# Kernel optimization log

Hardware: AMD Instinct MI355X
Metric: run time of the kernel (lower is better)

The kernel has to match this reference:

```python
import jax, jax.numpy as jnp
import numpy as np

EPSILON = float(np.finfo(np.float32).tiny)
K = 32                 # self.k
TRAIN_ENSEMBLE = 2     # repeat_sample in train mode
TAU = 0.1


def setup_inputs() -> dict:
    key = jax.random.key(0)
    scores = jax.random.normal(key, (256, 8192, 4), dtype=jnp.float32)  # [bsz, Nmax, ensemble]
    return {"scores": scores}


def reference(scores):
    bsz, Nmax, ensemble = scores.shape
    repeat = TRAIN_ENSEMBLE
    local_k = min(K, Nmax)

    # flat_scores: (bsz*ensemble, Nmax), then repeated over samples -> (repeat*bsz*ensemble, Nmax)
    flat = scores.transpose(0, 2, 1).reshape(bsz * ensemble, Nmax)
    flat = jnp.tile(flat, (repeat, 1))

    # Gumbel(0,1) noise (m.sample())
    g = jax.random.gumbel(jax.random.key(42), flat.shape, dtype=flat.dtype)
    flat = flat + g

    zeros = jnp.zeros_like(flat)

    def step(carry, _):
        f, khot, onehot = carry
        khot_mask = jnp.maximum(1.0 - onehot, EPSILON)
        f = f + jnp.log(khot_mask)
        onehot = jax.nn.softmax(f / TAU, axis=1)
        return (f, khot + onehot, onehot), None

    (_, khot, _), _ = jax.lax.scan(step, (flat, zeros, zeros), None, length=local_k)

    # hard top-k straight-through
    _, ind = jax.lax.top_k(khot, local_k)                      # (R, local_k)
    rows = jnp.arange(khot.shape[0])[:, None]
    khot_hard = jnp.zeros_like(khot).at[rows, ind].set(1.0)
    res = khot_hard - jax.lax.stop_gradient(khot) + khot

    # (repeat, bsz, ensemble, Nmax) -> (repeat, bsz, Nmax, ensemble)
    new_mask = res.reshape(repeat, bsz, ensemble, Nmax).transpose(0, 1, 3, 2)
    return new_mask
```

## Files before the change

kernel.cpp:

```cpp
#include <hip/hip_runtime.h>

#define TPB 256
#define ROWN 8192
#define CMAX 1024
#define EPS_TINY 1.1754943508222875e-38f

__device__ __forceinline__ unsigned rotl32(unsigned x, int r) {
  return (x << r) | (x >> (32 - r));
}

__device__ __forceinline__ unsigned tf_pxor(unsigned idx) {
  const unsigned ks0 = 0u, ks1 = 42u, ks2 = 0x1BD11BDAu ^ 0u ^ 42u;
  unsigned x0 = ks0;
  unsigned x1 = idx + ks1;
#define TF4(a,b,cc,d) \
  x0 += x1; x1 = rotl32(x1,(a));  x1 ^= x0; \
  x0 += x1; x1 = rotl32(x1,(b));  x1 ^= x0; \
  x0 += x1; x1 = rotl32(x1,(cc)); x1 ^= x0; \
  x0 += x1; x1 = rotl32(x1,(d));  x1 ^= x0;
  TF4(13,15,26,6)   x0 += ks1; x1 += ks2 + 1u;
  TF4(17,29,16,24)  x0 += ks2; x1 += ks0 + 2u;
  TF4(13,15,26,6)   x0 += ks0; x1 += ks1 + 3u;
  TF4(17,29,16,24)  x0 += ks1; x1 += ks2 + 4u;
  TF4(13,15,26,6)   x0 += ks2; x1 += ks0 + 5u;
#undef TF4
  return x0 ^ x1;
}

__device__ __forceinline__ float gumbel_of(unsigned idx) {
  const unsigned bits = tf_pxor(idx);
  float u = __uint_as_float((bits >> 9) | 0x3f800000u) - 1.0f;
  u = u + EPS_TINY;
  u = fmaxf(EPS_TINY, u);
  return -logf(-logf(u));
}

__device__ __forceinline__ float approx_gumbel(unsigned bits) {
  float u = __uint_as_float((bits >> 9) | 0x3f800000u) - 1.0f;
  u = u + EPS_TINY;
  u = fmaxf(EPS_TINY, u);
  float t;
  if (u >= 0.75f) {
    const float v = 1.0f - u;
    t = v * (1.0f + v * (0.5f + v * (0.33333334f + v * (0.25f + v * 0.2f))));
  } else {
    t = -0.69314718f * __log2f(u);
  }
  return -0.69314718f * __log2f(t);
}

__device__ __forceinline__ unsigned key16_of(float x) {
  const unsigned b = __float_as_uint(x) >> 16;
  return (b & 0x8000u) ? (0xFFFFu & ~b) : (b | 0x8000u);
}

__global__ __launch_bounds__(TPB, 8)
void topk_row(const void* __restrict__ scores_raw, int* __restrict__ selws) {
  const int t    = threadIdx.x;
  const int lane = t & 63;
  const int wave = t >> 6;

  const int i   = blockIdx.x;
  const int xcd = i & 7;
  const int k   = i >> 3;
  const int e   = k & 3;
  const int q   = k >> 2;
  const int b   = xcd * 32 + (q & 31);
  const int rep = q >> 5;
  const int r   = rep * 1024 + b * 4 + e;
  const unsigned gbase = (unsigned)r * (unsigned)ROWN;

  __shared__ unsigned       kLds[16][TPB];
  __shared__ unsigned short candIdx[CMAX];
  __shared__ float redM[2][4];
  __shared__ float redZ[2][4];
  __shared__ int   wtot[13][4];
  __shared__ int   f32flag;

  if (t == 0) f32flag = 0;
  __syncthreads();
  {
    const unsigned* w = (const unsigned*)scores_raw;
    bool bad = false;
#pragma unroll
    for (int p = 0; p < 4; ++p) {
      const unsigned x = w[t + 256 * p];
      const float flo = __uint_as_float((x & 0xFFFFu) << 16);
      const float fhi = __uint_as_float(x & 0xFFFF0000u);
      if (!(fabsf(flo) <= 16.0f) || !(fabsf(fhi) <= 16.0f)) bad = true;
    }
    if (bad) f32flag = 1;
  }
  __syncthreads();
  const bool in_f32 = (f32flag != 0);

  const size_t ebase0 = ((size_t)b * ROWN + (size_t)t) * 4 + (size_t)e;
  float m = -3.4e38f;
  {
    unsigned pair = 0u;
    if (in_f32) {
      const float* sp = (const float*)scores_raw;
#pragma unroll
      for (int j = 0; j < 32; ++j) {
        const float fj = sp[ebase0 + (size_t)(256 * j) * 4]
                       + approx_gumbel(tf_pxor(gbase + (unsigned)(t + 256 * j)));
        m = fmaxf(m, fj);
        const unsigned kk = key16_of(fj);
        if (j & 1) { pair |= kk << 16; kLds[j >> 1][t] = pair; }
        else pair = kk;
      }
    } else {
      const unsigned short* sp = (const unsigned short*)scores_raw;
#pragma unroll
      for (int j = 0; j < 32; ++j) {
        const float fj = __uint_as_float(((unsigned)sp[ebase0 + (size_t)(256 * j) * 4]) << 16)
                       + approx_gumbel(tf_pxor(gbase + (unsigned)(t + 256 * j)));
        m = fmaxf(m, fj);
        const unsigned kk = key16_of(fj);
        if (j & 1) { pair |= kk << 16; kLds[j >> 1][t] = pair; }
        else pair = kk;
      }
    }
  }

#pragma unroll
  for (int off = 32; off >= 1; off >>= 1) m = fmaxf(m, __shfl_xor(m, off));
  if (lane == 0) redM[0][wave] = m;
  __syncthreads();
  m = fmaxf(fmaxf(redM[0][0], redM[0][1]), fmaxf(redM[0][2], redM[0][3]));

  float lo = m - 25.0f, hi = m;
#pragma unroll 1
  for (int itb = 0; itb < 7; ++itb) {
    const float mid = 0.5f * (lo + hi);
    const unsigned kmid = key16_of(mid);
    int c = 0;
#pragma unroll
    for (int h = 0; h < 16; ++h) {
      const unsigned w = kLds[h][t];
      c += ((w & 0xFFFFu) > kmid) ? 1 : 0;
      c += ((w >> 16) > kmid) ? 1 : 0;
    }
#pragma unroll
    for (int off = 32; off >= 1; off >>= 1) c += __shfl_xor(c, off);
    if (lane == 0) wtot[itb][wave] = c;
    __syncthreads();
    const int tot = wtot[itb][0] + wtot[itb][1] + wtot[itb][2] + wtot[itb][3];
    if (tot >= 33) lo = mid; else hi = mid;
  }
  const float theta = lo - 2.34f;
  const unsigned ktheta = key16_of(theta);

  int cj = 0;
#pragma unroll
  for (int h = 0; h < 16; ++h) {
    const unsigned w = kLds[h][t];
    cj += ((w & 0xFFFFu) >= ktheta) ? 1 : 0;
    cj += ((w >> 16) >= ktheta) ? 1 : 0;
  }
  int incv = cj;
#pragma unroll
  for (int off = 1; off < 64; off <<= 1) {
    const int v = __shfl_up(incv, off);
    if (lane >= off) incv += v;
  }
  if (lane == 63) wtot[12][wave] = incv;
  __syncthreads();
  int base = 0;
  for (int w = 0; w < wave; ++w) base += wtot[12][w];
  int cnt = wtot[12][0] + wtot[12][1] + wtot[12][2] + wtot[12][3];
  if (cnt > CMAX) cnt = CMAX;
  int o = base + incv - cj;
#pragma unroll
  for (int h = 0; h < 16; ++h) {
    const unsigned w = kLds[h][t];
    if ((w & 0xFFFFu) >= ktheta) {
      if (o < CMAX) candIdx[o] = (unsigned short)(t + 256 * (2 * h));
      ++o;
    }
    if ((w >> 16) >= ktheta) {
      if (o < CMAX) candIdx[o] = (unsigned short)(t + 256 * (2 * h + 1));
      ++o;
    }
  }
  __syncthreads();

  float cfr[4], khr[4];
#pragma unroll
  for (int p = 0; p < 4; ++p) {
    cfr[p] = -3.0e38f; khr[p] = -3.0e38f;
    if (256 * p < cnt) {
      const int ci = t + 256 * p;
      if (ci < cnt) {
        const int n = (int)candIdx[ci];
        const size_t ei = ((size_t)b * ROWN + (size_t)n) * 4 + (size_t)e;
        float sc;
        if (in_f32) sc = ((const float*)scores_raw)[ei];
        else sc = __uint_as_float(((unsigned)((const unsigned short*)scores_raw)[ei]) << 16);
        cfr[p] = sc + gumbel_of(gbase + (unsigned)n);
        khr[p] = 0.0f;
      }
    }
  }

  float m2;
  {
    float mm = -3.4e38f;
#pragma unroll
    for (int p = 0; p < 4; ++p)
      if (256 * p < cnt) mm = fmaxf(mm, cfr[p]);
#pragma unroll
    for (int off = 32; off >= 1; off >>= 1) mm = fmaxf(mm, __shfl_xor(mm, off));
    if (lane == 0) redM[1][wave] = mm;
    __syncthreads();
    m2 = fmaxf(fmaxf(redM[1][0], redM[1][1]), fmaxf(redM[1][2], redM[1][3]));
  }

#pragma unroll 1
  for (int it = 0; it < 32; ++it) {
    float ek[4];
    float Z = 0.0f;
#pragma unroll
    for (int p = 0; p < 4; ++p) {
      float ev = 0.0f;
      if (256 * p < cnt) {
        ev = __expf((cfr[p] - m2) * 10.0f);
        Z += ev;
      }
      ek[p] = ev;
    }
#pragma unroll
    for (int off = 32; off >= 1; off >>= 1) Z += __shfl_xor(Z, off);
    if (lane == 0) redZ[it & 1][wave] = Z;

    const bool refresh = ((it & 3) == 2);
    if (refresh) {
      float mm = -3.4e38f;
#pragma unroll
      for (int p = 0; p < 4; ++p)
        if (256 * p < cnt) mm = fmaxf(mm, cfr[p]);
#pragma unroll
      for (int off = 32; off >= 1; off >>= 1) mm = fmaxf(mm, __shfl_xor(mm, off));
      if (lane == 0) redM[(it >> 2) & 1][wave] = mm;
    }
    __syncthreads();
    Z = (redZ[it & 1][0] + redZ[it & 1][1]) + (redZ[it & 1][2] + redZ[it & 1][3]);
    float m2n = m2;
    if (refresh) {
      const int bm = (it >> 2) & 1;
      m2n = fmaxf(fmaxf(redM[bm][0], redM[bm][1]), fmaxf(redM[bm][2], redM[bm][3]));
    }

    const float rz = __builtin_amdgcn_rcpf(Z);
#pragma unroll
    for (int p = 0; p < 4; ++p) {
      if (256 * p < cnt) {
        const float pp = ek[p] * rz;
        khr[p] += pp;
        cfr[p] += __logf(fmaxf(1.0f - pp, EPS_TINY));
      }
    }
    m2 = m2n;
  }

  float* khLds = (float*)&kLds[0][0];
#pragma unroll
  for (int p = 0; p < 4; ++p) {
    if (256 * p < cnt) {
      const int ci = t + 256 * p;
      if (ci < cnt) khLds[ci] = khr[p];
    }
  }
  __syncthreads();
  if (wave != 0) return;

  const int nch = (cnt + 63) >> 6;
#pragma unroll 1
  for (int pass = 0; pass < 32; ++pass) {
    float bv = -3.4e38f; int bn = 0x7FFFFFFF; int bci = 0;
#pragma unroll 1
    for (int c = 0; c < nch; ++c) {
      const int ci = lane + 64 * c;
      if (ci < cnt) {
        const float v = khLds[ci];
        const int  n = (int)candIdx[ci];
        if (v > bv || (v == bv && n < bn)) { bv = v; bn = n; bci = ci; }
      }
    }
#pragma unroll
    for (int off = 32; off >= 1; off >>= 1) {
      const float ov = __shfl_xor(bv, off);
      const int   on = __shfl_xor(bn, off);
      const int   oc = __shfl_xor(bci, off);
      if (ov > bv || (ov == bv && on < bn)) { bv = ov; bn = on; bci = oc; }
    }
    if (lane == 0) {
      selws[r * 32 + pass] = bn;
      khLds[bci] = -3.0e38f;
    }
  }
}

__global__ __launch_bounds__(TPB)
void expand_out(const int* __restrict__ selws, float4* __restrict__ out4) {
  const int t   = threadIdx.x;
  const int blk = blockIdx.x;
  const int grp = blk >> 2;
  const int s   = blk & 3;
  const int rep = grp >> 8;
  const int b   = grp & 255;

  __shared__ unsigned ebm[4 * 256];
#pragma unroll
  for (int p = 0; p < 4; ++p) ebm[t + 256 * p] = 0u;
  __syncthreads();
  if (t < 4) {
    const int r = rep * 1024 + b * 4 + t;
#pragma unroll 1
    for (int p = 0; p < 32; ++p) {
      const int ix = selws[r * 32 + p];
      ebm[t * 256 + (ix >> 5)] |= (1u << (ix & 31));
    }
  }
  __syncthreads();

  const size_t obase = (size_t)grp * ROWN;
#pragma unroll
  for (int j = 0; j < 8; ++j) {
    const int n = s * 2048 + t + 256 * j;
    float4 v;
    v.x = ((ebm[0 * 256 + (n >> 5)] >> (n & 31)) & 1u) ? 1.0f : 0.0f;
    v.y = ((ebm[1 * 256 + (n >> 5)] >> (n & 31)) & 1u) ? 1.0f : 0.0f;
    v.z = ((ebm[2 * 256 + (n >> 5)] >> (n & 31)) & 1u) ? 1.0f : 0.0f;
    v.w = ((ebm[3 * 256 + (n >> 5)] >> (n & 31)) & 1u) ? 1.0f : 0.0f;
    out4[obase + (size_t)n] = v;
  }
}

extern "C" void kernel_launch(void* const* d_in, const int* in_sizes, int n_in,
                              void* d_out, int out_size, void* d_ws, size_t ws_size,
                              hipStream_t stream) {
  const void* scores = d_in[0];
  int* selws = (int*)d_ws;
  topk_row<<<dim3(2048), dim3(TPB), 0, stream>>>(scores, selws);
  expand_out<<<dim3(2048), dim3(TPB), 0, stream>>>(selws, (float4*)d_out);
}
```

Before: 227.9 us.

## Parallelize final top-32 selection across all waves with two-level merge

```diff
diff --git a/kernel.cpp b/kernel.cpp
--- a/kernel.cpp
+++ b/kernel.cpp
@@ -263,41 +263,60 @@
     m2 = m2n;
   }
 
-  float* khLds = (float*)&kLds[0][0];
+  float*    selV = (float*)&kLds[0][0];
+  unsigned* selN = &kLds[1][0];
+
+  int idn[4];
 #pragma unroll
   for (int p = 0; p < 4; ++p) {
-    if (256 * p < cnt) {
-      const int ci = t + 256 * p;
-      if (ci < cnt) khLds[ci] = khr[p];
-    }
-  }
-  __syncthreads();
-  if (wave != 0) return;
-
-  const int nch = (cnt + 63) >> 6;
+    const int ci = t + 256 * p;
+    idn[p] = (256 * p < cnt && ci < cnt) ? (int)candIdx[ci] : 0x7FFFFFFF;
+  }
+
 #pragma unroll 1
   for (int pass = 0; pass < 32; ++pass) {
-    float bv = -3.4e38f; int bn = 0x7FFFFFFF; int bci = 0;
-#pragma unroll 1
-    for (int c = 0; c < nch; ++c) {
-      const int ci = lane + 64 * c;
-      if (ci < cnt) {
-        const float v = khLds[ci];
-        const int  n = (int)candIdx[ci];
-        if (v > bv || (v == bv && n < bn)) { bv = v; bn = n; bci = ci; }
+    float bv = -3.4e38f; int bn = 0x7FFFFFFF;
+#pragma unroll
+    for (int p = 0; p < 4; ++p) {
+      if (256 * p < cnt) {
+        const float v = khr[p]; const int n = idn[p];
+        if (v > bv || (v == bv && n < bn)) { bv = v; bn = n; }
       }
     }
 #pragma unroll
     for (int off = 32; off >= 1; off >>= 1) {
       const float ov = __shfl_xor(bv, off);
       const int   on = __shfl_xor(bn, off);
-      const int   oc = __shfl_xor(bci, off);
-      if (ov > bv || (ov == bv && on < bn)) { bv = ov; bn = on; bci = oc; }
-    }
-    if (lane == 0) {
-      selws[r * 32 + pass] = bn;
-      khLds[bci] = -3.0e38f;
-    }
+      if (ov > bv || (ov == bv && on < bn)) { bv = ov; bn = on; }
+    }
+    if (lane == 0) { selV[wave * 32 + pass] = bv; selN[wave * 32 + pass] = (unsigned)bn; }
+#pragma unroll
+    for (int p = 0; p < 4; ++p)
+      if (256 * p < cnt && idn[p] == bn) khr[p] = -3.0e38f;
+  }
+  __syncthreads();
+  if (wave != 0) return;
+
+  float mv[2]; int mn[2];
+#pragma unroll
+  for (int c = 0; c < 2; ++c) { mv[c] = selV[lane + 64 * c]; mn[c] = (int)selN[lane + 64 * c]; }
+#pragma unroll 1
+  for (int pass = 0; pass < 32; ++pass) {
+    float bv = -3.4e38f; int bn = 0x7FFFFFFF;
+#pragma unroll
+    for (int c = 0; c < 2; ++c) {
+      if (mv[c] > bv || (mv[c] == bv && mn[c] < bn)) { bv = mv[c]; bn = mn[c]; }
+    }
+#pragma unroll
+    for (int off = 32; off >= 1; off >>= 1) {
+      const float ov = __shfl_xor(bv, off);
+      const int   on = __shfl_xor(bn, off);
+      if (ov > bv || (ov == bv && on < bn)) { bv = ov; bn = on; }
+    }
+    if (lane == 0) selws[r * 32 + pass] = bn;
+#pragma unroll
+    for (int c = 0; c < 2; ++c)
+      if (mn[c] == bn) mv[c] = -3.0e38f;
   }
 }
 
```

Result: slower. 236.7 us (+3.8%).
